# Kernel tuning notes

Measured on AMD Instinct MI355X. Metric: run time of the kernel, lower is better.

## Reference

```python
import jax, jax.numpy as jnp
import numpy as np

B, CIN, COUT, N, K = 4, 64, 64, 16384, 8


def setup_inputs() -> dict:
    key = jax.random.key(0)
    k1, k2, k3, k4, k5 = jax.random.split(key, 5)
    features = jax.random.normal(k1, (B, CIN, N), dtype=jnp.float32)
    neighborhood = jax.random.randint(k2, (B, K, N), 0, N, dtype=jnp.int32)
    positions = jax.random.uniform(k3, (B, 3, N), dtype=jnp.float32)
    # learned parameters (kaiming-uniform-ish init)
    lim_t = np.sqrt(6.0 / CIN)
    weight_theta = jax.random.uniform(k4, (3, CIN, COUT), dtype=jnp.float32,
                                      minval=-lim_t, maxval=lim_t)
    weight_bias = jax.random.uniform(k5, (CIN, COUT), dtype=jnp.float32,
                                     minval=-lim_t, maxval=lim_t)
    bias = jnp.zeros((COUT,), dtype=jnp.float32)
    return {"features": features, "weight_theta": weight_theta,
            "weight_bias": weight_bias, "neighborhood": neighborhood,
            "positions": positions, "bias": bias}


def reference(features, weight_theta, weight_bias, neighborhood, positions, bias):
    # features: [B, Cin, N]; positions: [B, 3, N]; neighborhood: [B, K, N]
    Bv, Cin, Nv = features.shape
    Kv = neighborhood.shape[1]
    # gather neighbor positions: pos_j[b,d,k,n] = positions[b,d, nbh[b,k,n]]
    pos_j = jnp.take_along_axis(positions[:, :, None, :],
                                neighborhood[:, None, :, :].astype(jnp.int32),
                                axis=3)                        # [B,3,K,N]
    delta = pos_j - positions[:, :, None, :]                   # [B,3,K,N]
    # position-dependent linear weight applied to center features:
    # contrib[b,k,o,n] = sum_d delta[b,d,k,n] * (theta.f)[b,d,o,n] + (wb.f)[b,o,n]
    ft = jnp.einsum('dio,bin->bdon', weight_theta, features)   # [B,3,Cout,N]
    fb = jnp.einsum('io,bin->bon', weight_bias, features)      # [B,Cout,N]
    contrib = jnp.einsum('bdkn,bdon->bkon', delta, ft) + fb[:, None]  # [B,K,Cout,N]

    def scatter_b(contrib_b, idx_b):
        # contrib_b: [K,Cout,N], idx_b: [K,N]
        data = contrib_b.transpose(0, 2, 1).reshape(-1, contrib_b.shape[1])  # [K*N, Cout]
        ids = idx_b.reshape(-1)
        return jax.ops.segment_sum(data, ids, num_segments=Nv).T  # [Cout, N]

    out = jax.vmap(scatter_b)(contrib, neighborhood)           # [B,Cout,N]
    return out + bias[None, :, None]
```

## Files before the change

kernel.cpp:

```cpp
#include <hip/hip_runtime.h>
#include <hip/hip_fp16.h>

#define B_    4
#define CIN_  64
#define COUT_ 64
#define N_    16384
#define K_    8
#define CAP_  16

#define EDGES_PER_B (K_ * N_)
#define TOT_EDGES   (B_ * EDGES_PER_B)


__device__ __forceinline__ unsigned pack_h2(float a, float b) {
    return (unsigned)__half_as_ushort(__float2half(a))
         | ((unsigned)__half_as_ushort(__float2half(b)) << 16);
}

__device__ __forceinline__ float edge_dot(uint2 v, float qx, float qy, float qz) {
    const float f0 = __half2float(__ushort_as_half((unsigned short)(v.x)));
    const float f1 = __half2float(__ushort_as_half((unsigned short)(v.x >> 16)));
    const float f2 = __half2float(__ushort_as_half((unsigned short)(v.y)));
    const float f3 = __half2float(__ushort_as_half((unsigned short)(v.y >> 16)));
    return fmaf(qx, f0, fmaf(qy, f1, fmaf(qz, f2, f3)));
}

__global__ __launch_bounds__(512, 4) void fc_contribD(
    const float* __restrict__ feat,
    const float* __restrict__ theta,
    const float* __restrict__ wbias,
    const int*   __restrict__ nbh,
    const float* __restrict__ pos,
    int*         __restrict__ cursor,
    int*         __restrict__ bucket,
    uint2*       __restrict__ ftfb,
    float*       __restrict__ ws2)
{
    __shared__ uint2 Wl[CIN_ * COUT_];
    __shared__ float Fl[CIN_ * 64];

    const int tid  = threadIdx.x;
    const int lane = tid & 63;
    const int w    = tid >> 6;

    const int blocks_per_b = N_ / 128;
    const int b     = blockIdx.x / blocks_per_b;
    const int nbase = (blockIdx.x % blocks_per_b) * 128;

    for (int e = tid; e < CIN_ * COUT_; e += 512) {
        const int i = e >> 6, o = e & 63;
        const float wx = theta[0 * CIN_ * COUT_ + i * COUT_ + o];
        const float wy = theta[1 * CIN_ * COUT_ + i * COUT_ + o];
        const float wz = theta[2 * CIN_ * COUT_ + i * COUT_ + o];
        const float wb = wbias[i * COUT_ + o];
        uint2 u;
        u.x = pack_h2(wx, wy);
        u.y = pack_h2(wz, wb);
        Wl[e] = u;
    }

    const float* featb = feat + (size_t)b * CIN_ * N_;
    const float* posb  = pos  + (size_t)b * 3 * N_;
    const int*   nbhb  = nbh  + (size_t)b * K_ * N_;
    int*         curb  = cursor + b * N_;
    int*         bkb   = bucket + (size_t)b * N_ * CAP_;
    uint2*       fbb   = ftfb + ((size_t)b * N_ << 6);
    float*       ws2b  = ws2 + ((size_t)b * N_ << 6);

    for (int t = 0; t < 2; ++t) {
        const int n0 = nbase + t * 64;
        const int nn = w * 8;

        __syncthreads();
        for (int r = 0; r < 8; ++r) {
            const int i = r * 8 + w;
            Fl[i * 64 + lane] = featb[(size_t)i * N_ + n0 + lane];
        }

        const int pe = lane >> 3;
        const int ke = lane & 7;
        const int ne = n0 + nn + pe;
        const int je = nbhb[ke * N_ + ne];
        const int sle = atomicAdd(&curb[je], 1);
        if (sle < CAP_) bkb[je * CAP_ + sle] = ne;

        __syncthreads();

        float4 acc[8];
        #pragma unroll
        for (int j = 0; j < 8; ++j) acc[j] = make_float4(0.f, 0.f, 0.f, 0.f);

        #pragma unroll 2
        for (int i = 0; i < CIN_; ++i) {
            const uint2 wp = Wl[i * 64 + lane];
            const float2 w01 = __half22float2(*reinterpret_cast<const __half2*>(&wp.x));
            const float2 w23 = __half22float2(*reinterpret_cast<const __half2*>(&wp.y));
            const float4 fA = *(const float4*)&Fl[i * 64 + nn];
            const float4 fB = *(const float4*)&Fl[i * 64 + nn + 4];
            const float fs[8] = {fA.x, fA.y, fA.z, fA.w, fB.x, fB.y, fB.z, fB.w};
            #pragma unroll
            for (int j = 0; j < 8; ++j) {
                acc[j].x = fmaf(w01.x, fs[j], acc[j].x);
                acc[j].y = fmaf(w01.y, fs[j], acc[j].y);
                acc[j].z = fmaf(w23.x, fs[j], acc[j].z);
                acc[j].w = fmaf(w23.y, fs[j], acc[j].w);
            }
        }

        const unsigned long long ovf = __ballot(sle >= CAP_);

        #pragma unroll
        for (int p = 0; p < 8; ++p) {
            const int n = n0 + nn + p;
            const float px = posb[0 * N_ + n];
            const float py = posb[1 * N_ + n];
            const float pz = posb[2 * N_ + n];
            float4 a = acc[p];
            a.w = fmaf(-px, a.x, fmaf(-py, a.y, fmaf(-pz, a.z, a.w)));

            uint2 v;
            v.x = pack_h2(a.x, a.y);
            v.y = pack_h2(a.z, a.w);
            fbb[((size_t)n << 6) + lane] = v;

            const unsigned m8 = (unsigned)((ovf >> (p * 8)) & 0xFFull);
            if (m8) {
                #pragma unroll
                for (int k = 0; k < 8; ++k) {
                    if ((m8 >> k) & 1) {
                        const int src = p * 8 + k;
                        const int jt = __shfl(je, src);
                        const float qx = posb[jt];
                        const float qy = posb[N_ + jt];
                        const float qz = posb[2 * N_ + jt];
                        const float c = fmaf(qx, a.x,
                                        fmaf(qy, a.y,
                                        fmaf(qz, a.z, a.w)));
                        atomicAdd(&ws2b[((size_t)jt << 6) + lane], c);
                    }
                }
            }
        }
    }
}

__global__ __launch_bounds__(512, 4) void fc_gatherD(
    const uint2* __restrict__ ftfb,
    const int*   __restrict__ bucket,
    const int*   __restrict__ cursor,
    const float* __restrict__ ws2,
    const float* __restrict__ pos,
    const float* __restrict__ bias,
    float*       __restrict__ out)
{
    __shared__ float T[64][65];
    const int tid  = threadIdx.x;
    const int lane = tid & 63;
    const int w    = tid >> 6;

    const int tiles_per_b = N_ / 64;
    const int b  = blockIdx.x / tiles_per_b;
    const int n0 = (blockIdx.x % tiles_per_b) * 64;

    const uint2* fbb  = ftfb + ((size_t)b * N_ << 6);
    const int*   bkb  = bucket + (size_t)b * N_ * CAP_;
    const float* posb = pos + (size_t)b * 3 * N_;
    const float* ws2b = ws2 + ((size_t)b * N_ << 6);

    for (int g = 0; g < 8; ++g) {
        const int jj = w * 8 + g;
        const int j  = n0 + jj;
        const int cnt_tot = cursor[b * N_ + j];
        const int cnt = cnt_tot < CAP_ ? cnt_tot : CAP_;
        const float qx = posb[j];
        const float qy = posb[N_ + j];
        const float qz = posb[2 * N_ + j];

        const int myidx = (lane < cnt) ? bkb[j * CAP_ + lane] : 0;

        float acc = (cnt_tot > CAP_) ? ws2b[((size_t)j << 6) + lane] : 0.f;

        int e = 0;
        for (; e + 8 <= cnt; e += 8) {
            int m[8];
            #pragma unroll
            for (int q = 0; q < 8; ++q) m[q] = __shfl(myidx, e + q);
            uint2 v[8];
            #pragma unroll
            for (int q = 0; q < 8; ++q) v[q] = fbb[((size_t)m[q] << 6) + lane];
            #pragma unroll
            for (int q = 0; q < 8; ++q) acc += edge_dot(v[q], qx, qy, qz);
        }
        for (; e + 4 <= cnt; e += 4) {
            const int m0 = __shfl(myidx, e + 0);
            const int m1 = __shfl(myidx, e + 1);
            const int m2 = __shfl(myidx, e + 2);
            const int m3 = __shfl(myidx, e + 3);
            const uint2 v0 = fbb[((size_t)m0 << 6) + lane];
            const uint2 v1 = fbb[((size_t)m1 << 6) + lane];
            const uint2 v2 = fbb[((size_t)m2 << 6) + lane];
            const uint2 v3 = fbb[((size_t)m3 << 6) + lane];
            acc += edge_dot(v0, qx, qy, qz);
            acc += edge_dot(v1, qx, qy, qz);
            acc += edge_dot(v2, qx, qy, qz);
            acc += edge_dot(v3, qx, qy, qz);
        }
        for (; e < cnt; ++e) {
            const int m = __shfl(myidx, e);
            const uint2 v = fbb[((size_t)m << 6) + lane];
            acc += edge_dot(v, qx, qy, qz);
        }
        T[jj][lane] = acc;
    }
    __syncthreads();

    float* outb = out + (size_t)b * COUT_ * N_;
    for (int r = 0; r < 8; ++r) {
        const int o = r * 8 + w;
        outb[(size_t)o * N_ + n0 + lane] = T[lane][o] + bias[o];
    }
}

__global__ __launch_bounds__(256) void flexconv_main(
    const float* __restrict__ feat,
    const float* __restrict__ theta,
    const float* __restrict__ wbias,
    const int*   __restrict__ nbh,
    const float* __restrict__ pos,
    float*       __restrict__ ws)
{
    __shared__ float4 Wl[CIN_ * COUT_];
    __shared__ float  Fl[CIN_ * 64];

    const int tid  = threadIdx.x;
    const int lane = tid & 63;
    const int w    = tid >> 6;

    const int blocks_per_b = N_ / 128;
    const int b     = blockIdx.x / blocks_per_b;
    const int nbase = (blockIdx.x % blocks_per_b) * 128;

    for (int e = tid; e < CIN_ * COUT_; e += 256) {
        const int i = e >> 6, o = e & 63;
        float4 wv;
        wv.x = theta[0 * CIN_ * COUT_ + i * COUT_ + o];
        wv.y = theta[1 * CIN_ * COUT_ + i * COUT_ + o];
        wv.z = theta[2 * CIN_ * COUT_ + i * COUT_ + o];
        wv.w = wbias[i * COUT_ + o];
        Wl[e] = wv;
    }

    const float* featb = feat + (size_t)b * CIN_ * N_;
    const float* posb  = pos  + (size_t)b * 3 * N_;
    const int*   nbhb  = nbh  + (size_t)b * K_ * N_;
    float*       wsb   = ws   + (size_t)b * N_ * COUT_;

    for (int t = 0; t < 2; ++t) {
        const int n0 = nbase + t * 64;

        __syncthreads();
        for (int r = 0; r < 16; ++r) {
            const int i = r * 4 + w;
            Fl[i * 64 + lane] = featb[(size_t)i * N_ + n0 + lane];
        }
        __syncthreads();

        for (int g = 0; g < 4; ++g) {
            const int nn = w * 16 + g * 4;
            float4 acc[4];
            #pragma unroll
            for (int j = 0; j < 4; ++j) acc[j] = make_float4(0.f, 0.f, 0.f, 0.f);

            #pragma unroll 8
            for (int i = 0; i < CIN_; ++i) {
                const float4 wv = Wl[i * 64 + lane];
                const float f0 = Fl[i * 64 + nn + 0];
                const float f1 = Fl[i * 64 + nn + 1];
                const float f2 = Fl[i * 64 + nn + 2];
                const float f3 = Fl[i * 64 + nn + 3];
                acc[0].x = fmaf(wv.x, f0, acc[0].x);
                acc[0].y = fmaf(wv.y, f0, acc[0].y);
                acc[0].z = fmaf(wv.z, f0, acc[0].z);
                acc[0].w = fmaf(wv.w, f0, acc[0].w);
                acc[1].x = fmaf(wv.x, f1, acc[1].x);
                acc[1].y = fmaf(wv.y, f1, acc[1].y);
                acc[1].z = fmaf(wv.z, f1, acc[1].z);
                acc[1].w = fmaf(wv.w, f1, acc[1].w);
                acc[2].x = fmaf(wv.x, f2, acc[2].x);
                acc[2].y = fmaf(wv.y, f2, acc[2].y);
                acc[2].z = fmaf(wv.z, f2, acc[2].z);
                acc[2].w = fmaf(wv.w, f2, acc[2].w);
                acc[3].x = fmaf(wv.x, f3, acc[3].x);
                acc[3].y = fmaf(wv.y, f3, acc[3].y);
                acc[3].z = fmaf(wv.z, f3, acc[3].z);
                acc[3].w = fmaf(wv.w, f3, acc[3].w);
            }

            #pragma unroll
            for (int j = 0; j < 4; ++j) {
                const int n = n0 + nn + j;
                const float px = posb[0 * N_ + n];
                const float py = posb[1 * N_ + n];
                const float pz = posb[2 * N_ + n];
                const float4 a = acc[j];
                #pragma unroll
                for (int k = 0; k < K_; ++k) {
                    const int idx = nbhb[k * N_ + n];
                    const float dx = posb[0 * N_ + idx] - px;
                    const float dy = posb[1 * N_ + idx] - py;
                    const float dz = posb[2 * N_ + idx] - pz;
                    const float c  = fmaf(dx, a.x, fmaf(dy, a.y, fmaf(dz, a.z, a.w)));
                    atomicAdd(&wsb[(size_t)idx * COUT_ + lane], c);
                }
            }
        }
    }
}

__global__ __launch_bounds__(256) void flexconv_finish(
    const float* __restrict__ ws,
    const float* __restrict__ bias,
    float*       __restrict__ out)
{
    __shared__ float T[64][65];
    const int tid  = threadIdx.x;
    const int lane = tid & 63;
    const int w    = tid >> 6;

    const int tiles_per_b = N_ / 64;
    const int b  = blockIdx.x / tiles_per_b;
    const int n0 = (blockIdx.x % tiles_per_b) * 64;

    const float* wsb = ws + (size_t)b * N_ * COUT_;
    for (int r = 0; r < 16; ++r) {
        const int nn = r * 4 + w;
        T[nn][lane] = wsb[(size_t)(n0 + nn) * COUT_ + lane];
    }
    __syncthreads();

    float* outb = out + (size_t)b * COUT_ * N_;
    for (int r = 0; r < 16; ++r) {
        const int o = r * 4 + w;
        outb[(size_t)o * N_ + n0 + lane] = T[lane][o] + bias[o];
    }
}

extern "C" void kernel_launch(void* const* d_in, const int* in_sizes, int n_in,
                              void* d_out, int out_size, void* d_ws, size_t ws_size,
                              hipStream_t stream) {
    const float* features = (const float*)d_in[0];
    const float* theta    = (const float*)d_in[1];
    const float* wbias    = (const float*)d_in[2];
    const int*   nbh      = (const int*)  d_in[3];
    const float* pos      = (const float*)d_in[4];
    const float* bias     = (const float*)d_in[5];
    float* out = (float*)d_out;

    {
        const size_t ftfb_bytes   = ((size_t)B_ * N_ << 6) * sizeof(uint2);
        const size_t bucket_bytes = (size_t)B_ * N_ * CAP_ * sizeof(int);
        const size_t cursor_bytes = (size_t)B_ * N_ * sizeof(int);
        const size_t ws2_bytes    = ((size_t)B_ * N_ << 6) * sizeof(float);

        size_t off = 0;
        uint2* ftfb   = (uint2*)((char*)d_ws + off); off += ftfb_bytes;
        int*   bucket = (int*)  ((char*)d_ws + off); off += bucket_bytes;
        int*   cursor = (int*)  ((char*)d_ws + off); off += cursor_bytes;
        float* ws2    = (float*)((char*)d_ws + off); off += ws2_bytes;

        if (ws_size >= off) {
            hipMemsetAsync(cursor, 0, cursor_bytes + ws2_bytes, stream);
            fc_contribD<<<B_ * (N_ / 128), 512, 0, stream>>>(features, theta, wbias,
                                                             nbh, pos, cursor,
                                                             bucket, ftfb, ws2);
            fc_gatherD<<<B_ * (N_ / 64), 512, 0, stream>>>(ftfb, bucket, cursor,
                                                           ws2, pos, bias, out);
            return;
        }
    }

    {
        float* ws = (float*)d_ws;
        const size_t ws_bytes = (size_t)B_ * N_ * COUT_ * sizeof(float);
        hipMemsetAsync(ws, 0, ws_bytes, stream);
        flexconv_main<<<B_ * (N_ / 128), 256, 0, stream>>>(features, theta, wbias,
                                                           nbh, pos, ws);
        flexconv_finish<<<B_ * (N_ / 64), 256, 0, stream>>>(ws, bias, out);
    }
}
```

Before: 163.5 us.

## Push per-edge contributions into destination slots instead of gathering per-node coefficients

```diff
diff --git a/kernel.cpp b/kernel.cpp
--- a/kernel.cpp
+++ b/kernel.cpp
@@ -6,11 +6,13 @@
 #define COUT_ 64
 #define N_    16384
 #define K_    8
-#define CAP_  16
+#define CAPF_ 12
+#define CAPD_ 16
 
 #define EDGES_PER_B (K_ * N_)
 #define TOT_EDGES   (B_ * EDGES_PER_B)
 
+struct h4 { __half2 lo, hi; };
 
 __device__ __forceinline__ unsigned pack_h2(float a, float b) {
     return (unsigned)__half_as_ushort(__float2half(a))
@@ -24,6 +26,196 @@
     const float f3 = __half2float(__ushort_as_half((unsigned short)(v.y >> 16)));
     return fmaf(qx, f0, fmaf(qy, f1, fmaf(qz, f2, f3)));
 }
+
+
+__global__ __launch_bounds__(256) void fc_recB(
+    const int*   __restrict__ nbh,
+    const float* __restrict__ pos,
+    int*         __restrict__ cursor,
+    float4*      __restrict__ rec)
+{
+    const int gid = blockIdx.x * 256 + threadIdx.x;
+    const int b   = gid >> 14;
+    const int n   = gid & (N_ - 1);
+
+    const int*   nbhb = nbh + (size_t)b * K_ * N_;
+    const float* posb = pos + (size_t)b * 3 * N_;
+    float4*      recb = rec + ((size_t)b * N_ + n) * K_;
+
+    #pragma unroll
+    for (int k = 0; k < K_; ++k) {
+        const int j   = nbhb[k * N_ + n];
+        const int sle = atomicAdd(&cursor[b * N_ + j], 1);
+        const int slot = (sle < CAPF_) ? (j * CAPF_ + sle) : -(j + 1);
+        recb[k] = make_float4(posb[j], posb[N_ + j], posb[2 * N_ + j],
+                              __int_as_float(slot));
+    }
+}
+
+__global__ __launch_bounds__(512, 4) void fc_contribF(
+    const float*  __restrict__ feat,
+    const float*  __restrict__ theta,
+    const float*  __restrict__ wbias,
+    const float4* __restrict__ rec,
+    const float*  __restrict__ pos,
+    __half*       __restrict__ cval,
+    float*        __restrict__ ws2)
+{
+    __shared__ float4 Wl[CIN_ * COUT_];
+    __shared__ float  Fl[CIN_ * 64];
+
+    const int tid  = threadIdx.x;
+    const int lane = tid & 63;
+    const int w    = tid >> 6;
+
+    const int blocks_per_b = N_ / 128;
+    const int b     = blockIdx.x / blocks_per_b;
+    const int nbase = (blockIdx.x % blocks_per_b) * 128;
+
+    for (int e = tid; e < CIN_ * COUT_; e += 512) {
+        const int i = e >> 6, o = e & 63;
+        float4 wv;
+        wv.x = theta[0 * CIN_ * COUT_ + i * COUT_ + o];
+        wv.y = theta[1 * CIN_ * COUT_ + i * COUT_ + o];
+        wv.z = theta[2 * CIN_ * COUT_ + i * COUT_ + o];
+        wv.w = wbias[i * COUT_ + o];
+        Wl[e] = wv;
+    }
+
+    const float*  featb = feat + (size_t)b * CIN_ * N_;
+    const float*  posb  = pos  + (size_t)b * 3 * N_;
+    const float4* recb  = rec  + (size_t)b * N_ * K_;
+    __half*       cvb   = cval + (size_t)b * N_ * CAPF_ * 64;
+    float*        ws2b  = ws2 + ((size_t)b * N_ << 6);
+
+    for (int t = 0; t < 2; ++t) {
+        const int n0 = nbase + t * 64;
+
+        __syncthreads();
+        for (int r = 0; r < 8; ++r) {
+            const int i = r * 8 + w;
+            Fl[i * 64 + lane] = featb[(size_t)i * N_ + n0 + lane];
+        }
+        __syncthreads();
+
+        const int nn = w * 8;
+        float4 acc[8];
+        #pragma unroll
+        for (int j = 0; j < 8; ++j) acc[j] = make_float4(0.f, 0.f, 0.f, 0.f);
+
+        #pragma unroll 2
+        for (int i = 0; i < CIN_; ++i) {
+            const float4 wv = Wl[i * 64 + lane];
+            const float4 fA = *(const float4*)&Fl[i * 64 + nn];
+            const float4 fB = *(const float4*)&Fl[i * 64 + nn + 4];
+            const float fs[8] = {fA.x, fA.y, fA.z, fA.w, fB.x, fB.y, fB.z, fB.w};
+            #pragma unroll
+            for (int j = 0; j < 8; ++j) {
+                acc[j].x = fmaf(wv.x, fs[j], acc[j].x);
+                acc[j].y = fmaf(wv.y, fs[j], acc[j].y);
+                acc[j].z = fmaf(wv.z, fs[j], acc[j].z);
+                acc[j].w = fmaf(wv.w, fs[j], acc[j].w);
+            }
+        }
+
+        #pragma unroll
+        for (int j = 0; j < 8; ++j) {
+            const int n = n0 + nn + j;
+            const float px = posb[0 * N_ + n];
+            const float py = posb[1 * N_ + n];
+            const float pz = posb[2 * N_ + n];
+            float4 a = acc[j];
+            a.w = fmaf(-px, a.x, fmaf(-py, a.y, fmaf(-pz, a.z, a.w)));
+            #pragma unroll
+            for (int k = 0; k < K_; ++k) {
+                const float4 r = recb[(size_t)n * K_ + k];
+                const int slot = __float_as_int(r.w);
+                const float c  = fmaf(r.x, a.x, fmaf(r.y, a.y, fmaf(r.z, a.z, a.w)));
+                if (slot >= 0) {
+                    cvb[((size_t)slot << 6) + lane] = __float2half(c);
+                } else {
+                    atomicAdd(&ws2b[((size_t)(-slot - 1) << 6) + lane], c);
+                }
+            }
+        }
+    }
+}
+
+__global__ __launch_bounds__(512) void fc_gatherF(
+    const __half* __restrict__ cval,
+    const int*    __restrict__ cursor,
+    const float*  __restrict__ ws2,
+    const float*  __restrict__ bias,
+    float*        __restrict__ out)
+{
+    __shared__ float T[64][65];
+    __shared__ float V[64][65];
+    const int tid  = threadIdx.x;
+    const int lane = tid & 63;
+    const int w    = tid >> 6;
+
+    const int tiles_per_b = N_ / 64;
+    const int b  = blockIdx.x / tiles_per_b;
+    const int n0 = (blockIdx.x % tiles_per_b) * 64;
+
+    const __half* cvb  = cval + (size_t)b * N_ * CAPF_ * 64;
+    const h4*     cb4  = (const h4*)cvb;
+    const float*  ws2b = ws2 + ((size_t)b * N_ << 6);
+
+    for (int g = 0; g < 8; ++g) {
+        const int jj = w * 8 + g;
+        const int j  = n0 + jj;
+        const int cnt_tot = cursor[b * N_ + j];
+        const int cnt  = cnt_tot < CAPF_ ? cnt_tot : CAPF_;
+        const int base = j * CAPF_;
+
+        const h4* p4 = cb4 + ((size_t)base << 4) + (lane >> 4) * 16 + (lane & 15);
+        float2 sl = make_float2(0.f, 0.f);
+        float2 sh = make_float2(0.f, 0.f);
+        const int full = cnt >> 2;
+        int it = 0;
+        for (; it + 2 <= full; it += 2) {
+            const h4 a0 = p4[0];
+            const h4 a1 = p4[64];
+            float2 t0 = __half22float2(a0.lo), t1 = __half22float2(a1.lo);
+            sl.x += t0.x + t1.x; sl.y += t0.y + t1.y;
+            t0 = __half22float2(a0.hi); t1 = __half22float2(a1.hi);
+            sh.x += t0.x + t1.x; sh.y += t0.y + t1.y;
+            p4 += 128;
+        }
+        if (it < full) {
+            const h4 a0 = p4[0];
+            float2 t0 = __half22float2(a0.lo);
+            sl.x += t0.x; sl.y += t0.y;
+            t0 = __half22float2(a0.hi);
+            sh.x += t0.x; sh.y += t0.y;
+        }
+        sl.x += __shfl_xor(sl.x, 16); sl.y += __shfl_xor(sl.y, 16);
+        sh.x += __shfl_xor(sh.x, 16); sh.y += __shfl_xor(sh.y, 16);
+        sl.x += __shfl_xor(sl.x, 32); sl.y += __shfl_xor(sl.y, 32);
+        sh.x += __shfl_xor(sh.x, 32); sh.y += __shfl_xor(sh.y, 32);
+
+        float tail = (cnt_tot > CAPF_) ? ws2b[((size_t)j << 6) + lane] : 0.f;
+        const __half* pt = cvb + ((size_t)(base + (full << 2)) << 6) + lane;
+        for (int e = full << 2; e < cnt; ++e) { tail += __half2float(*pt); pt += 64; }
+
+        T[jj][lane] = tail;
+        if (lane < 16) {
+            V[jj][4 * lane + 0] = sl.x;
+            V[jj][4 * lane + 1] = sl.y;
+            V[jj][4 * lane + 2] = sh.x;
+            V[jj][4 * lane + 3] = sh.y;
+        }
+    }
+    __syncthreads();
+
+    float* outb = out + (size_t)b * COUT_ * N_;
+    for (int r = 0; r < 8; ++r) {
+        const int o = r * 8 + w;
+        outb[(size_t)o * N_ + n0 + lane] = T[lane][o] + V[lane][o] + bias[o];
+    }
+}
+
 
 __global__ __launch_bounds__(512, 4) void fc_contribD(
     const float* __restrict__ feat,
@@ -63,7 +255,7 @@
     const float* posb  = pos  + (size_t)b * 3 * N_;
     const int*   nbhb  = nbh  + (size_t)b * K_ * N_;
     int*         curb  = cursor + b * N_;
-    int*         bkb   = bucket + (size_t)b * N_ * CAP_;
+    int*         bkb   = bucket + (size_t)b * N_ * CAPD_;
     uint2*       fbb   = ftfb + ((size_t)b * N_ << 6);
     float*       ws2b  = ws2 + ((size_t)b * N_ << 6);
 
@@ -82,7 +274,7 @@
         const int ne = n0 + nn + pe;
         const int je = nbhb[ke * N_ + ne];
         const int sle = atomicAdd(&curb[je], 1);
-        if (sle < CAP_) bkb[je * CAP_ + sle] = ne;
+        if (sle < CAPD_) bkb[je * CAPD_ + sle] = ne;
 
         __syncthreads();
 
@@ -107,7 +299,7 @@
             }
         }
 
-        const unsigned long long ovf = __ballot(sle >= CAP_);
+        const unsigned long long ovf = __ballot(sle >= CAPD_);
 
         #pragma unroll
         for (int p = 0; p < 8; ++p) {
@@ -163,7 +355,7 @@
     const int n0 = (blockIdx.x % tiles_per_b) * 64;
 
     const uint2* fbb  = ftfb + ((size_t)b * N_ << 6);
-    const int*   bkb  = bucket + (size_t)b * N_ * CAP_;
+    const int*   bkb  = bucket + (size_t)b * N_ * CAPD_;
     const float* posb = pos + (size_t)b * 3 * N_;
     const float* ws2b = ws2 + ((size_t)b * N_ << 6);
 
@@ -171,14 +363,13 @@
         const int jj = w * 8 + g;
         const int j  = n0 + jj;
         const int cnt_tot = cursor[b * N_ + j];
-        const int cnt = cnt_tot < CAP_ ? cnt_tot : CAP_;
+        const int cnt = cnt_tot < CAPD_ ? cnt_tot : CAPD_;
         const float qx = posb[j];
         const float qy = posb[N_ + j];
         const float qz = posb[2 * N_ + j];
 
-        const int myidx = (lane < cnt) ? bkb[j * CAP_ + lane] : 0;
-
-        float acc = (cnt_tot > CAP_) ? ws2b[((size_t)j << 6) + lane] : 0.f;
+        const int myidx = (lane < cnt) ? bkb[j * CAPD_ + lane] : 0;
+        float acc = (cnt_tot > CAPD_) ? ws2b[((size_t)j << 6) + lane] : 0.f;
 
         int e = 0;
         for (; e + 8 <= cnt; e += 8) {
@@ -356,11 +547,33 @@
     const float* bias     = (const float*)d_in[5];
     float* out = (float*)d_out;
 
+    const size_t cursor_bytes = (size_t)B_ * N_ * sizeof(int);
+    const size_t ws2_bytes    = ((size_t)B_ * N_ << 6) * sizeof(float);
+
+    {
+        const size_t cval_bytes = (size_t)B_ * N_ * CAPF_ * 64 * sizeof(__half);
+        const size_t rec_bytes  = (size_t)TOT_EDGES * sizeof(float4);
+
+        size_t off = 0;
+        __half* cval   = (__half*)((char*)d_ws + off); off += cval_bytes;
+        int*    cursor = (int*)   ((char*)d_ws + off); off += cursor_bytes;
+        float*  ws2    = (float*) ((char*)d_ws + off); off += ws2_bytes;
+        float4* rec    = (float4*)((char*)d_ws + off); off += rec_bytes;
+
+        if (ws_size >= off) {
+            hipMemsetAsync(cursor, 0, cursor_bytes + ws2_bytes, stream);
+            fc_recB<<<(B_ * N_) / 256, 256, 0, stream>>>(nbh, pos, cursor, rec);
+            fc_contribF<<<B_ * (N_ / 128), 512, 0, stream>>>(features, theta, wbias,
+                                                             rec, pos, cval, ws2);
+            fc_gatherF<<<B_ * (N_ / 64), 512, 0, stream>>>(cval, cursor, ws2,
+                                                           bias, out);
+            return;
+        }
+    }
+
     {
         const size_t ftfb_bytes   = ((size_t)B_ * N_ << 6) * sizeof(uint2);
-        const size_t bucket_bytes = (size_t)B_ * N_ * CAP_ * sizeof(int);
-        const size_t cursor_bytes = (size_t)B_ * N_ * sizeof(int);
-        const size_t ws2_bytes    = ((size_t)B_ * N_ << 6) * sizeof(float);
+        const size_t bucket_bytes = (size_t)B_ * N_ * CAPD_ * sizeof(int);
 
         size_t off = 0;
         uint2* ftfb   = (uint2*)((char*)d_ws + off); off += ftfb_bytes;
```

After: 182.5 us. 1.12x slower.
